# Kernel tuning notes

Measured on AMD Instinct MI355X. Metric: run time of the kernel, lower is better.

Reference implementation:

```python
import jax, jax.numpy as jnp
import numpy as np

T = 256          # tokens
H = 1024         # hidden_size
E = 64           # num_experts
I = 512          # routed intermediate_size
SI = 2048        # shared_expert_intermediate_size
TOP_K = 6
N_GROUP = 8
TOPK_GROUP = 4
ROUTED_SCALE = 2.5


def setup_inputs() -> dict:
    key = jax.random.key(0)
    ks = jax.random.split(key, 9)
    s = 0.02
    return {
        "hidden_states": jax.random.normal(ks[0], (T, H), jnp.float32),
        "gate_w": jax.random.normal(ks[1], (E, H), jnp.float32) * s,
        "e_bias": jax.random.normal(ks[2], (E,), jnp.float32) * 0.01,
        "w1": jax.random.normal(ks[3], (E, I, H), jnp.float32) * s,  # gate proj
        "w3": jax.random.normal(ks[4], (E, I, H), jnp.float32) * s,  # up proj
        "w2": jax.random.normal(ks[5], (E, H, I), jnp.float32) * s,  # down proj
        "ws_gate": jax.random.normal(ks[6], (SI, H), jnp.float32) * s,
        "ws_up": jax.random.normal(ks[7], (SI, H), jnp.float32) * s,
        "ws_down": jax.random.normal(ks[8], (H, SI), jnp.float32) * s,
    }


def _noaux_tc_routing(logits, e_bias):
    # DeepSeek-V3 group-limited sigmoid routing (is_thop=False path).
    scores = jax.nn.sigmoid(logits)                         # [T, E]
    swb = scores + e_bias                                   # bias only picks experts
    t, e = scores.shape
    g = swb.reshape(t, N_GROUP, e // N_GROUP)
    group_scores = jax.lax.top_k(g, 2)[0].sum(-1)           # top-2 sum per group [T, G]
    _, gidx = jax.lax.top_k(group_scores, TOPK_GROUP)
    gmask = jax.nn.one_hot(gidx, N_GROUP, dtype=scores.dtype).sum(-2)  # [T, G]
    smask = jnp.repeat(gmask, e // N_GROUP, axis=-1)        # [T, E]
    _, tidx = jax.lax.top_k(swb * smask, TOP_K)
    nmask = jax.nn.one_hot(tidx, e, dtype=scores.dtype).sum(-2)
    s = scores * nmask
    s = s / (s.sum(-1, keepdims=True) + 1e-20) * ROUTED_SCALE  # [T, E], TOP_K nonzeros
    # torch code returns topk(values, indices) of s; s itself is the dense
    # combine-weight matrix with exactly those values scattered at the indices.
    return s


def reference(hidden_states, gate_w, e_bias, w1, w3, w2, ws_gate, ws_up, ws_down):
    x = hidden_states
    # gate: cublas_mm with fp32 output
    logits = (x @ gate_w.T).astype(jnp.float32)             # [T, E]
    cw = _noaux_tc_routing(logits, e_bias)                  # [T, E] combine weights

    # routed experts: gated MLP per expert, combined by routing weights
    h1 = jnp.einsum('th,eih->tei', x, w1)
    h3 = jnp.einsum('th,eih->tei', x, w3)
    act = jax.nn.silu(h1) * h3                              # [T, E, I]
    eo = jnp.einsum('tei,ehi->teh', act, w2)                # [T, E, H]
    routed = jnp.einsum('teh,te->th', eo, cw.astype(x.dtype))

    # shared experts: GatedMLP
    shared = (jax.nn.silu(x @ ws_gate.T) * (x @ ws_up.T)) @ ws_down.T

    return shared + routed
```

## Files before the change

kernel.cpp:

```cpp
#include <hip/hip_runtime.h>
#include <math.h>

#define T_TOK 256
#define H_DIM 1024
#define E_NUM 64
#define I_DIM 512
#define SI_DIM 2048

#define BN 64
#define BM 32

typedef __attribute__((ext_vector_type(8))) short short8;
typedef __attribute__((ext_vector_type(8))) __bf16 bf16x8;
typedef __attribute__((ext_vector_type(4))) float floatx4;
typedef __attribute__((ext_vector_type(4))) unsigned short ushort4v;
typedef __attribute__((ext_vector_type(8))) unsigned short ushort8;

static __device__ __forceinline__ unsigned short f2bf(float f) {
  unsigned u = __float_as_uint(f);
  u += 0x7FFFu + ((u >> 16) & 1u);
  return (unsigned short)(u >> 16);
}

static __device__ __forceinline__ ushort4v pack4(floatx4 v) {
  ushort4v b;
  b[0] = f2bf(v[0]); b[1] = f2bf(v[1]); b[2] = f2bf(v[2]); b[3] = f2bf(v[3]);
  return b;
}

static __device__ __forceinline__ bf16x8 pack8(floatx4 a, floatx4 b) {
  ushort8 s;
  s[0] = f2bf(a[0]); s[1] = f2bf(a[1]); s[2] = f2bf(a[2]); s[3] = f2bf(a[3]);
  s[4] = f2bf(b[0]); s[5] = f2bf(b[1]); s[6] = f2bf(b[2]); s[7] = f2bf(b[3]);
  union { ushort8 u; bf16x8 v; } cv; cv.u = s;
  return cv.v;
}

static __device__ __forceinline__ floatx4 mfma16(bf16x8 a, bf16x8 b, floatx4 c) {
  return __builtin_amdgcn_mfma_f32_16x16x32_bf16(a, b, c, 0, 0, 0);
}

__global__ __launch_bounds__(256) void gate_route_kernel(
    const float* __restrict__ x, const float* __restrict__ gw,
    const float* __restrict__ ebias, unsigned short* __restrict__ xbf,
    int* __restrict__ cnt, int* __restrict__ tok_list,
    float* __restrict__ wt_list) {
  const int t = blockIdx.x;
  const int j = threadIdx.x;
  __shared__ float xs[H_DIM];
  __shared__ double pd[4 * 64];

  floatx4 v = ((const floatx4*)(x + (size_t)t * H_DIM))[j];
  xs[4 * j + 0] = v[0]; xs[4 * j + 1] = v[1];
  xs[4 * j + 2] = v[2]; xs[4 * j + 3] = v[3];
  ((ushort4v*)(xbf + (size_t)t * H_DIM))[j] = pack4(v);
  __syncthreads();

  const int e = j & 63, ch = j >> 6;
  const float* wr = gw + (size_t)e * H_DIM + ch * 256;
  const float* xc = xs + ch * 256;
  double acc = 0.0;
  for (int i = 0; i < 64; ++i) {
    floatx4 w = ((const floatx4*)wr)[i];
    acc += (double)xc[4 * i + 0] * (double)w[0]
         + (double)xc[4 * i + 1] * (double)w[1]
         + (double)xc[4 * i + 2] * (double)w[2]
         + (double)xc[4 * i + 3] * (double)w[3];
  }
  pd[ch * 64 + e] = acc;
  __syncthreads();

  if (j < 64) {
    const int lane = j;
    const double logit = pd[lane] + pd[64 + lane] + pd[128 + lane] + pd[192 + lane];
    const double score = 1.0 / (1.0 + exp(-logit));
    const double swb = score + (double)ebias[lane];

    double m1 = swb, m2 = -1.0e300;
    #pragma unroll
    for (int d = 1; d < 8; d <<= 1) {
      double o1 = __shfl_xor(m1, d);
      double o2 = __shfl_xor(m2, d);
      double hi = fmax(m1, o1), lo = fmin(m1, o1);
      m1 = hi;
      m2 = fmax(lo, fmax(m2, o2));
    }
    const double gscore = m1 + m2;

    double gs[8];
    #pragma unroll
    for (int g = 0; g < 8; ++g) gs[g] = __shfl(gscore, g << 3);
    unsigned gsel = 0;
    #pragma unroll
    for (int it = 0; it < 4; ++it) {
      int best = 0; double bv = -1.0e300;
      #pragma unroll
      for (int g = 0; g < 8; ++g) {
        bool taken = (gsel >> g) & 1u;
        if (!taken && gs[g] > bv) { bv = gs[g]; best = g; }
      }
      gsel |= 1u << best;
    }

    double key = ((gsel >> (lane >> 3)) & 1u) ? swb : -1.0e300;
    int selected = 0;
    for (int it = 0; it < 6; ++it) {
      double vv = key; int idx = lane;
      #pragma unroll
      for (int d = 1; d < 64; d <<= 1) {
        double ov = __shfl_xor(vv, d);
        int oi = __shfl_xor(idx, d);
        if (ov > vv || (ov == vv && oi < idx)) { vv = ov; idx = oi; }
      }
      if (lane == idx) { selected = 1; key = -1.0e300; }
    }

    double ssum = selected ? score : 0.0;
    #pragma unroll
    for (int d = 1; d < 64; d <<= 1) ssum += __shfl_xor(ssum, d);

    if (selected) {
      float wgt = (float)(score / (ssum + 1e-20) * 2.5);
      int p = atomicAdd(&cnt[lane], 1);
      tok_list[lane * T_TOK + p] = t;
      wt_list[lane * T_TOK + p] = wgt;
    }
  }
}

__global__ __launch_bounds__(256, 2) void routed_gu_kernel(
    const unsigned short* __restrict__ xbf, const float* __restrict__ w1,
    const float* __restrict__ w3, const int* __restrict__ cnt,
    const int* __restrict__ tok_list, unsigned short* __restrict__ act_r) {
  __shared__ __align__(16) char sAB[BM * 1024];

  const int e = blockIdx.x >> 3;
  const int n0 = (blockIdx.x & 7) * BN;
  const int j = threadIdx.x;
  const int wv = j >> 6, lane = j & 63;
  const int q = lane >> 4, c = lane & 15;
  const int kq = q * 8;
  const int ne = cnt[e];
  if (ne <= 0) return;
  const int* tl = tok_list + e * T_TOK;
  unsigned short* ap = act_r + (size_t)e * T_TOK * I_DIM;

  const float* wgR = w1 + ((size_t)e * I_DIM + n0 + wv * 16 + c) * H_DIM;
  const float* wuR = w3 + ((size_t)e * I_DIM + n0 + wv * 16 + c) * H_DIM;

  const int sr = j >> 3, st8 = (j & 7) * 8;
  const int xrs = (sr & 7) << 4;
  const int xr0 = (c & 7) << 4;

  for (int m0 = 0; m0 < ne; m0 += BM) {
    const int tok = (m0 + sr < ne) ? tl[m0 + sr] : tl[m0];
    const unsigned short* aRow = xbf + (size_t)tok * H_DIM;

    floatx4 cg0 = *(const floatx4*)(wgR + kq);
    floatx4 cg1 = *(const floatx4*)(wgR + kq + 4);
    floatx4 cu0 = *(const floatx4*)(wuR + kq);
    floatx4 cu1 = *(const floatx4*)(wuR + kq + 4);

    floatx4 ag0 = (floatx4)0.0f, ag1 = (floatx4)0.0f;
    floatx4 au0 = (floatx4)0.0f, au1 = (floatx4)0.0f;

    for (int half = 0; half < 2; ++half) {
      const int kbase = half * 512;
      __syncthreads();
      #pragma unroll
      for (int i = 0; i < 512; i += 64) {
        const int col = st8 + i;
        *(bf16x8*)(sAB + sr * 1024 + ((2 * col) ^ xrs)) =
            *(const bf16x8*)(aRow + kbase + col);
      }
      __syncthreads();
      for (int kcl = 0; kcl < 512; kcl += 32) {
        const int kc = kbase + kcl;
        bf16x8 bg = pack8(cg0, cg1);
        bf16x8 bu = pack8(cu0, cu1);
        if (kc + 32 < H_DIM) {
          cg0 = *(const floatx4*)(wgR + kc + 32 + kq);
          cg1 = *(const floatx4*)(wgR + kc + 32 + kq + 4);
          cu0 = *(const floatx4*)(wuR + kc + 32 + kq);
          cu1 = *(const floatx4*)(wuR + kc + 32 + kq + 4);
        }
        const int kb = 2 * (kcl + kq);
        bf16x8 a0 = *(const bf16x8*)(sAB + c * 1024 + (kb ^ xr0));
        bf16x8 a1 = *(const bf16x8*)(sAB + (16 + c) * 1024 + (kb ^ xr0));
        ag0 = mfma16(a0, bg, ag0);
        ag1 = mfma16(a1, bg, ag1);
        au0 = mfma16(a0, bu, au0);
        au1 = mfma16(a1, bu, au1);
      }
    }
    #pragma unroll
    for (int s = 0; s < 2; ++s) {
      floatx4 g = s ? ag1 : ag0;
      floatx4 u = s ? au1 : au0;
      #pragma unroll
      for (int r = 0; r < 4; ++r) {
        const int m = m0 + s * 16 + q * 4 + r;
        if (m < ne) {
          float gg = g[r], uu = u[r];
          float a = gg / (1.0f + __expf(-gg)) * uu;
          ap[(size_t)m * I_DIM + n0 + wv * 16 + c] = f2bf(a);
        }
      }
    }
  }
}

__global__ __launch_bounds__(256, 2) void shared_gu_kernel(
    const unsigned short* __restrict__ xbf, const float* __restrict__ wsg,
    const float* __restrict__ wsu, unsigned short* __restrict__ act_s) {
  __shared__ __align__(16) char sAB[BM * 1024];

  const int n0 = (blockIdx.x & 31) * BN;
  const int m0 = (blockIdx.x >> 5) * BM;
  const int j = threadIdx.x;
  const int wv = j >> 6, lane = j & 63;
  const int q = lane >> 4, c = lane & 15;
  const int kq = q * 8;

  const float* wgR = wsg + (size_t)(n0 + wv * 16 + c) * H_DIM;
  const float* wuR = wsu + (size_t)(n0 + wv * 16 + c) * H_DIM;

  const int sr = j >> 3, st8 = (j & 7) * 8;
  const int xrs = (sr & 7) << 4;
  const int xr0 = (c & 7) << 4;
  const unsigned short* aRow = xbf + (size_t)(m0 + sr) * H_DIM;

  floatx4 cg0 = *(const floatx4*)(wgR + kq);
  floatx4 cg1 = *(const floatx4*)(wgR + kq + 4);
  floatx4 cu0 = *(const floatx4*)(wuR + kq);
  floatx4 cu1 = *(const floatx4*)(wuR + kq + 4);

  floatx4 ag0 = (floatx4)0.0f, ag1 = (floatx4)0.0f;
  floatx4 au0 = (floatx4)0.0f, au1 = (floatx4)0.0f;

  for (int half = 0; half < 2; ++half) {
    const int kbase = half * 512;
    __syncthreads();
    #pragma unroll
    for (int i = 0; i < 512; i += 64) {
      const int col = st8 + i;
      *(bf16x8*)(sAB + sr * 1024 + ((2 * col) ^ xrs)) =
          *(const bf16x8*)(aRow + kbase + col);
    }
    __syncthreads();
    for (int kcl = 0; kcl < 512; kcl += 32) {
      const int kc = kbase + kcl;
      bf16x8 bg = pack8(cg0, cg1);
      bf16x8 bu = pack8(cu0, cu1);
      if (kc + 32 < H_DIM) {
        cg0 = *(const floatx4*)(wgR + kc + 32 + kq);
        cg1 = *(const floatx4*)(wgR + kc + 32 + kq + 4);
        cu0 = *(const floatx4*)(wuR + kc + 32 + kq);
        cu1 = *(const floatx4*)(wuR + kc + 32 + kq + 4);
      }
      const int kb = 2 * (kcl + kq);
      bf16x8 a0 = *(const bf16x8*)(sAB + c * 1024 + (kb ^ xr0));
      bf16x8 a1 = *(const bf16x8*)(sAB + (16 + c) * 1024 + (kb ^ xr0));
      ag0 = mfma16(a0, bg, ag0);
      ag1 = mfma16(a1, bg, ag1);
      au0 = mfma16(a0, bu, au0);
      au1 = mfma16(a1, bu, au1);
    }
  }
  #pragma unroll
  for (int s = 0; s < 2; ++s) {
    floatx4 g = s ? ag1 : ag0;
    floatx4 u = s ? au1 : au0;
    #pragma unroll
    for (int r = 0; r < 4; ++r) {
      const int m = m0 + s * 16 + q * 4 + r;
      float gg = g[r], uu = u[r];
      float a = gg / (1.0f + __expf(-gg)) * uu;
      act_s[(size_t)m * SI_DIM + n0 + wv * 16 + c] = f2bf(a);
    }
  }
}

__global__ __launch_bounds__(256, 2) void shared_down_kernel(
    const unsigned short* __restrict__ act_s, const float* __restrict__ wsd,
    float* __restrict__ out) {
  __shared__ __align__(16) char sAB[BM * 1024];

  const int n0 = (blockIdx.x & 15) * BN;
  const int m0 = ((blockIdx.x >> 4) & 7) * BM;
  const int kh = blockIdx.x >> 7;
  const int kbeg = kh * (SI_DIM / 2);
  const int j = threadIdx.x;
  const int wv = j >> 6, lane = j & 63;
  const int q = lane >> 4, c = lane & 15;
  const int kq = q * 8;

  const float* wR = wsd + (size_t)(n0 + wv * 16 + c) * SI_DIM + kbeg;

  const int sr = j >> 3, st8 = (j & 7) * 8;
  const int xrs = (sr & 7) << 4;
  const int xr0 = (c & 7) << 4;
  const unsigned short* aRow = act_s + (size_t)(m0 + sr) * SI_DIM + kbeg;

  floatx4 cw0 = *(const floatx4*)(wR + kq);
  floatx4 cw1 = *(const floatx4*)(wR + kq + 4);

  floatx4 ac0 = (floatx4)0.0f, ac1 = (floatx4)0.0f;
  for (int half = 0; half < 2; ++half) {
    const int kbase = half * 512;
    __syncthreads();
    #pragma unroll
    for (int i = 0; i < 512; i += 64) {
      const int col = st8 + i;
      *(bf16x8*)(sAB + sr * 1024 + ((2 * col) ^ xrs)) =
          *(const bf16x8*)(aRow + kbase + col);
    }
    __syncthreads();
    for (int kcl = 0; kcl < 512; kcl += 32) {
      const int kc = kbase + kcl;
      bf16x8 b = pack8(cw0, cw1);
      if (kc + 32 < SI_DIM / 2) {
        cw0 = *(const floatx4*)(wR + kc + 32 + kq);
        cw1 = *(const floatx4*)(wR + kc + 32 + kq + 4);
      }
      const int kb = 2 * (kcl + kq);
      bf16x8 a0 = *(const bf16x8*)(sAB + c * 1024 + (kb ^ xr0));
      bf16x8 a1 = *(const bf16x8*)(sAB + (16 + c) * 1024 + (kb ^ xr0));
      ac0 = mfma16(a0, b, ac0);
      ac1 = mfma16(a1, b, ac1);
    }
  }
  #pragma unroll
  for (int s = 0; s < 2; ++s) {
    floatx4 d = s ? ac1 : ac0;
    #pragma unroll
    for (int r = 0; r < 4; ++r) {
      const int m = m0 + s * 16 + q * 4 + r;
      atomicAdd(&out[(size_t)m * H_DIM + n0 + wv * 16 + c], d[r]);
    }
  }
}

__global__ __launch_bounds__(256, 2) void routed_down_kernel(
    const unsigned short* __restrict__ act_r, const float* __restrict__ w2,
    const int* __restrict__ cnt, const int* __restrict__ tok_list,
    const float* __restrict__ wt_list, float* __restrict__ out) {
  __shared__ __align__(16) char sAB[BM * 1024];

  const int e = blockIdx.x >> 4;
  const int n0 = (blockIdx.x & 15) * BN;
  const int j = threadIdx.x;
  const int wv = j >> 6, lane = j & 63;
  const int q = lane >> 4, c = lane & 15;
  const int kq = q * 8;
  const int ne = cnt[e];
  if (ne <= 0) return;
  const int* tl = tok_list + e * T_TOK;
  const float* wl = wt_list + e * T_TOK;
  const unsigned short* apb = act_r + (size_t)e * T_TOK * I_DIM;
  const float* wR = w2 + ((size_t)e * H_DIM + n0 + wv * 16 + c) * I_DIM;

  const int sr = j >> 3, st8 = (j & 7) * 8;
  const int xrs = (sr & 7) << 4;
  const int xr0 = (c & 7) << 4;

  for (int m0 = 0; m0 < ne; m0 += BM) {
    __syncthreads();
    {
      int ar = m0 + sr;
      if (ar >= ne) ar = m0;
      const unsigned short* aRow = apb + (size_t)ar * I_DIM;
      #pragma unroll
      for (int i = 0; i < I_DIM; i += 64) {
        const int col = st8 + i;
        *(bf16x8*)(sAB + sr * 1024 + ((2 * col) ^ xrs)) =
            *(const bf16x8*)(aRow + col);
      }
    }
    __syncthreads();

    floatx4 cw0 = *(const floatx4*)(wR + kq);
    floatx4 cw1 = *(const floatx4*)(wR + kq + 4);

    floatx4 ac0 = (floatx4)0.0f, ac1 = (floatx4)0.0f;
    for (int kc = 0; kc < I_DIM; kc += 32) {
      bf16x8 b = pack8(cw0, cw1);
      if (kc + 32 < I_DIM) {
        cw0 = *(const floatx4*)(wR + kc + 32 + kq);
        cw1 = *(const floatx4*)(wR + kc + 32 + kq + 4);
      }
      const int kb = 2 * (kc + kq);
      bf16x8 a0 = *(const bf16x8*)(sAB + c * 1024 + (kb ^ xr0));
      bf16x8 a1 = *(const bf16x8*)(sAB + (16 + c) * 1024 + (kb ^ xr0));
      ac0 = mfma16(a0, b, ac0);
      ac1 = mfma16(a1, b, ac1);
    }
    #pragma unroll
    for (int s = 0; s < 2; ++s) {
      floatx4 d = s ? ac1 : ac0;
      #pragma unroll
      for (int r = 0; r < 4; ++r) {
        const int mi = s * 16 + q * 4 + r;
        if (m0 + mi < ne) {
          atomicAdd(&out[(size_t)tl[m0 + mi] * H_DIM + n0 + wv * 16 + c],
                    d[r] * wl[m0 + mi]);
        }
      }
    }
  }
}

extern "C" void kernel_launch(void* const* d_in, const int* in_sizes, int n_in,
                              void* d_out, int out_size, void* d_ws, size_t ws_size,
                              hipStream_t stream) {
  const float* x   = (const float*)d_in[0];
  const float* gw  = (const float*)d_in[1];
  const float* eb  = (const float*)d_in[2];
  const float* w1  = (const float*)d_in[3];
  const float* w3  = (const float*)d_in[4];
  const float* w2  = (const float*)d_in[5];
  const float* wsg = (const float*)d_in[6];
  const float* wsu = (const float*)d_in[7];
  const float* wsd = (const float*)d_in[8];
  float* out = (float*)d_out;

  char* ws = (char*)d_ws;
  unsigned short* xbf   = (unsigned short*)(ws);
  unsigned short* act_s = (unsigned short*)(ws + 524288);
  int*   cnt            = (int*)(ws + 1572864);
  int*   tok            = (int*)(ws + 1573120);
  float* wt             = (float*)(ws + 1638656);
  unsigned short* act_r = (unsigned short*)(ws + 1704192);

  hipMemsetAsync(cnt, 0, E_NUM * sizeof(int), stream);
  hipMemsetAsync(out, 0, (size_t)T_TOK * H_DIM * sizeof(float), stream);
  gate_route_kernel<<<dim3(T_TOK), dim3(256), 0, stream>>>(x, gw, eb, xbf, cnt, tok, wt);
  routed_gu_kernel<<<dim3(E_NUM * (I_DIM / BN)), dim3(256), 0, stream>>>(xbf, w1, w3, cnt, tok, act_r);
  shared_gu_kernel<<<dim3((SI_DIM / BN) * (T_TOK / BM)), dim3(256), 0, stream>>>(xbf, wsg, wsu, act_s);
  shared_down_kernel<<<dim3((H_DIM / BN) * (T_TOK / BM) * 2), dim3(256), 0, stream>>>(act_s, wsd, out);
  routed_down_kernel<<<dim3(E_NUM * (H_DIM / BN)), dim3(256), 0, stream>>>(act_r, w2, cnt, tok, wt, out);
}
```

Before: 480.6 us.

## Stage converted bf16 weight tiles in LDS and stream activations from global

```diff
diff --git a/kernel.cpp b/kernel.cpp
--- a/kernel.cpp
+++ b/kernel.cpp
@@ -6,15 +6,11 @@
 #define E_NUM 64
 #define I_DIM 512
 #define SI_DIM 2048
-
-#define BN 64
-#define BM 32
-
-typedef __attribute__((ext_vector_type(8))) short short8;
+#define TK 256
+
 typedef __attribute__((ext_vector_type(8))) __bf16 bf16x8;
 typedef __attribute__((ext_vector_type(4))) float floatx4;
 typedef __attribute__((ext_vector_type(4))) unsigned short ushort4v;
-typedef __attribute__((ext_vector_type(8))) unsigned short ushort8;
 
 static __device__ __forceinline__ unsigned short f2bf(float f) {
   unsigned u = __float_as_uint(f);
@@ -26,14 +22,6 @@
   ushort4v b;
   b[0] = f2bf(v[0]); b[1] = f2bf(v[1]); b[2] = f2bf(v[2]); b[3] = f2bf(v[3]);
   return b;
-}
-
-static __device__ __forceinline__ bf16x8 pack8(floatx4 a, floatx4 b) {
-  ushort8 s;
-  s[0] = f2bf(a[0]); s[1] = f2bf(a[1]); s[2] = f2bf(a[2]); s[3] = f2bf(a[3]);
-  s[4] = f2bf(b[0]); s[5] = f2bf(b[1]); s[6] = f2bf(b[2]); s[7] = f2bf(b[3]);
-  union { ushort8 u; bf16x8 v; } cv; cv.u = s;
-  return cv.v;
 }
 
 static __device__ __forceinline__ floatx4 mfma16(bf16x8 a, bf16x8 b, floatx4 c) {
@@ -128,14 +116,15 @@
   }
 }
 
-__global__ __launch_bounds__(256, 2) void routed_gu_kernel(
+__global__ __launch_bounds__(256, 4) void routed_gu_kernel(
     const unsigned short* __restrict__ xbf, const float* __restrict__ w1,
     const float* __restrict__ w3, const int* __restrict__ cnt,
     const int* __restrict__ tok_list, unsigned short* __restrict__ act_r) {
-  __shared__ __align__(16) char sAB[BM * 1024];
-
-  const int e = blockIdx.x >> 3;
-  const int n0 = (blockIdx.x & 7) * BN;
+  __shared__ __align__(16) char sW[2 * 32 * 512];
+
+  const int bid = blockIdx.x;
+  const int e = bid >> 4;
+  const int n0 = (bid & 15) * 32;
   const int j = threadIdx.x;
   const int wv = j >> 6, lane = j & 63;
   const int q = lane >> 4, c = lane & 15;
@@ -145,210 +134,190 @@
   const int* tl = tok_list + e * T_TOK;
   unsigned short* ap = act_r + (size_t)e * T_TOK * I_DIM;
 
-  const float* wgR = w1 + ((size_t)e * I_DIM + n0 + wv * 16 + c) * H_DIM;
-  const float* wuR = w3 + ((size_t)e * I_DIM + n0 + wv * 16 + c) * H_DIM;
-
-  const int sr = j >> 3, st8 = (j & 7) * 8;
-  const int xrs = (sr & 7) << 4;
-  const int xr0 = (c & 7) << 4;
-
-  for (int m0 = 0; m0 < ne; m0 += BM) {
-    const int tok = (m0 + sr < ne) ? tl[m0 + sr] : tl[m0];
-    const unsigned short* aRow = xbf + (size_t)tok * H_DIM;
-
-    floatx4 cg0 = *(const floatx4*)(wgR + kq);
-    floatx4 cg1 = *(const floatx4*)(wgR + kq + 4);
-    floatx4 cu0 = *(const floatx4*)(wuR + kq);
-    floatx4 cu1 = *(const floatx4*)(wuR + kq + 4);
-
-    floatx4 ag0 = (floatx4)0.0f, ag1 = (floatx4)0.0f;
-    floatx4 au0 = (floatx4)0.0f, au1 = (floatx4)0.0f;
-
-    for (int half = 0; half < 2; ++half) {
-      const int kbase = half * 512;
+  const float* w1g = w1 + ((size_t)e * I_DIM + n0) * H_DIM;
+  const float* w3g = w3 + ((size_t)e * I_DIM + n0) * H_DIM;
+  const int x0 = (c & 7) << 4;
+
+  for (int m0 = 0; m0 < ne; m0 += 64) {
+    int ti = m0 + wv * 16 + c; if (ti > ne - 1) ti = ne - 1;
+    const unsigned short* aP = xbf + (size_t)tl[ti] * H_DIM;
+
+    floatx4 ag0 = (floatx4)0.f, ag1 = (floatx4)0.f;
+    floatx4 au0 = (floatx4)0.f, au1 = (floatx4)0.f;
+
+    for (int kt = 0; kt < H_DIM; kt += TK) {
       __syncthreads();
       #pragma unroll
-      for (int i = 0; i < 512; i += 64) {
-        const int col = st8 + i;
-        *(bf16x8*)(sAB + sr * 1024 + ((2 * col) ^ xrs)) =
-            *(const bf16x8*)(aRow + kbase + col);
+      for (int b = 0; b < 2; ++b) {
+        floatx4 f[8];
+        #pragma unroll
+        for (int t = 0; t < 8; ++t) {
+          const int id = wv * 16 + b * 8 + t;
+          const float* base = (id < 32) ? w1g : w3g;
+          f[t] = *(const floatx4*)(base + (size_t)(id & 31) * H_DIM + kt + lane * 4);
+        }
+        #pragma unroll
+        for (int t = 0; t < 8; ++t) {
+          const int id = wv * 16 + b * 8 + t;
+          const int rl = id & 31;
+          *(ushort4v*)(sW + (id >> 5) * 16384 + rl * 512 +
+                       ((lane * 8) ^ ((rl & 7) << 4))) = pack4(f[t]);
+        }
       }
       __syncthreads();
-      for (int kcl = 0; kcl < 512; kcl += 32) {
-        const int kc = kbase + kcl;
-        bf16x8 bg = pack8(cg0, cg1);
-        bf16x8 bu = pack8(cu0, cu1);
-        if (kc + 32 < H_DIM) {
-          cg0 = *(const floatx4*)(wgR + kc + 32 + kq);
-          cg1 = *(const floatx4*)(wgR + kc + 32 + kq + 4);
-          cu0 = *(const floatx4*)(wuR + kc + 32 + kq);
-          cu1 = *(const floatx4*)(wuR + kc + 32 + kq + 4);
-        }
+      for (int kcl = 0; kcl < TK; kcl += 32) {
+        bf16x8 a = *(const bf16x8*)(aP + kt + kcl + kq);
         const int kb = 2 * (kcl + kq);
-        bf16x8 a0 = *(const bf16x8*)(sAB + c * 1024 + (kb ^ xr0));
-        bf16x8 a1 = *(const bf16x8*)(sAB + (16 + c) * 1024 + (kb ^ xr0));
-        ag0 = mfma16(a0, bg, ag0);
-        ag1 = mfma16(a1, bg, ag1);
-        au0 = mfma16(a0, bu, au0);
-        au1 = mfma16(a1, bu, au1);
-      }
-    }
-    #pragma unroll
-    for (int s = 0; s < 2; ++s) {
-      floatx4 g = s ? ag1 : ag0;
-      floatx4 u = s ? au1 : au0;
-      #pragma unroll
-      for (int r = 0; r < 4; ++r) {
-        const int m = m0 + s * 16 + q * 4 + r;
-        if (m < ne) {
-          float gg = g[r], uu = u[r];
-          float a = gg / (1.0f + __expf(-gg)) * uu;
-          ap[(size_t)m * I_DIM + n0 + wv * 16 + c] = f2bf(a);
-        }
-      }
-    }
-  }
-}
-
-__global__ __launch_bounds__(256, 2) void shared_gu_kernel(
+        bf16x8 bg0 = *(const bf16x8*)(sW + c * 512 + (kb ^ x0));
+        bf16x8 bg1 = *(const bf16x8*)(sW + (16 + c) * 512 + (kb ^ x0));
+        bf16x8 bu0 = *(const bf16x8*)(sW + 16384 + c * 512 + (kb ^ x0));
+        bf16x8 bu1 = *(const bf16x8*)(sW + 16384 + (16 + c) * 512 + (kb ^ x0));
+        ag0 = mfma16(a, bg0, ag0);
+        ag1 = mfma16(a, bg1, ag1);
+        au0 = mfma16(a, bu0, au0);
+        au1 = mfma16(a, bu1, au1);
+      }
+    }
+    #pragma unroll
+    for (int r = 0; r < 4; ++r) {
+      const int m = m0 + wv * 16 + q * 4 + r;
+      if (m < ne) {
+        float g0 = ag0[r], u0 = au0[r];
+        float g1 = ag1[r], u1 = au1[r];
+        ap[(size_t)m * I_DIM + n0 + c] = f2bf(g0 / (1.f + __expf(-g0)) * u0);
+        ap[(size_t)m * I_DIM + n0 + 16 + c] = f2bf(g1 / (1.f + __expf(-g1)) * u1);
+      }
+    }
+  }
+}
+
+__global__ __launch_bounds__(256, 4) void shared_gu_kernel(
     const unsigned short* __restrict__ xbf, const float* __restrict__ wsg,
     const float* __restrict__ wsu, unsigned short* __restrict__ act_s) {
-  __shared__ __align__(16) char sAB[BM * 1024];
-
-  const int n0 = (blockIdx.x & 31) * BN;
-  const int m0 = (blockIdx.x >> 5) * BM;
+  __shared__ __align__(16) char sW[2 * 32 * 512];
+
+  const int bid = blockIdx.x;
+  const int n0 = (bid & 63) * 32;
+  const int m0 = (bid >> 6) * 64;
   const int j = threadIdx.x;
   const int wv = j >> 6, lane = j & 63;
   const int q = lane >> 4, c = lane & 15;
   const int kq = q * 8;
 
-  const float* wgR = wsg + (size_t)(n0 + wv * 16 + c) * H_DIM;
-  const float* wuR = wsu + (size_t)(n0 + wv * 16 + c) * H_DIM;
-
-  const int sr = j >> 3, st8 = (j & 7) * 8;
-  const int xrs = (sr & 7) << 4;
-  const int xr0 = (c & 7) << 4;
-  const unsigned short* aRow = xbf + (size_t)(m0 + sr) * H_DIM;
-
-  floatx4 cg0 = *(const floatx4*)(wgR + kq);
-  floatx4 cg1 = *(const floatx4*)(wgR + kq + 4);
-  floatx4 cu0 = *(const floatx4*)(wuR + kq);
-  floatx4 cu1 = *(const floatx4*)(wuR + kq + 4);
-
-  floatx4 ag0 = (floatx4)0.0f, ag1 = (floatx4)0.0f;
-  floatx4 au0 = (floatx4)0.0f, au1 = (floatx4)0.0f;
-
-  for (int half = 0; half < 2; ++half) {
-    const int kbase = half * 512;
+  const float* wgg = wsg + (size_t)n0 * H_DIM;
+  const float* wug = wsu + (size_t)n0 * H_DIM;
+  const int x0 = (c & 7) << 4;
+  const unsigned short* aP = xbf + (size_t)(m0 + wv * 16 + c) * H_DIM;
+
+  floatx4 ag0 = (floatx4)0.f, ag1 = (floatx4)0.f;
+  floatx4 au0 = (floatx4)0.f, au1 = (floatx4)0.f;
+
+  for (int kt = 0; kt < H_DIM; kt += TK) {
     __syncthreads();
     #pragma unroll
-    for (int i = 0; i < 512; i += 64) {
-      const int col = st8 + i;
-      *(bf16x8*)(sAB + sr * 1024 + ((2 * col) ^ xrs)) =
-          *(const bf16x8*)(aRow + kbase + col);
+    for (int b = 0; b < 2; ++b) {
+      floatx4 f[8];
+      #pragma unroll
+      for (int t = 0; t < 8; ++t) {
+        const int id = wv * 16 + b * 8 + t;
+        const float* base = (id < 32) ? wgg : wug;
+        f[t] = *(const floatx4*)(base + (size_t)(id & 31) * H_DIM + kt + lane * 4);
+      }
+      #pragma unroll
+      for (int t = 0; t < 8; ++t) {
+        const int id = wv * 16 + b * 8 + t;
+        const int rl = id & 31;
+        *(ushort4v*)(sW + (id >> 5) * 16384 + rl * 512 +
+                     ((lane * 8) ^ ((rl & 7) << 4))) = pack4(f[t]);
+      }
     }
     __syncthreads();
-    for (int kcl = 0; kcl < 512; kcl += 32) {
-      const int kc = kbase + kcl;
-      bf16x8 bg = pack8(cg0, cg1);
-      bf16x8 bu = pack8(cu0, cu1);
-      if (kc + 32 < H_DIM) {
-        cg0 = *(const floatx4*)(wgR + kc + 32 + kq);
-        cg1 = *(const floatx4*)(wgR + kc + 32 + kq + 4);
-        cu0 = *(const floatx4*)(wuR + kc + 32 + kq);
-        cu1 = *(const floatx4*)(wuR + kc + 32 + kq + 4);
-      }
+    for (int kcl = 0; kcl < TK; kcl += 32) {
+      bf16x8 a = *(const bf16x8*)(aP + kt + kcl + kq);
       const int kb = 2 * (kcl + kq);
-      bf16x8 a0 = *(const bf16x8*)(sAB + c * 1024 + (kb ^ xr0));
-      bf16x8 a1 = *(const bf16x8*)(sAB + (16 + c) * 1024 + (kb ^ xr0));
-      ag0 = mfma16(a0, bg, ag0);
-      ag1 = mfma16(a1, bg, ag1);
-      au0 = mfma16(a0, bu, au0);
-      au1 = mfma16(a1, bu, au1);
+      bf16x8 bg0 = *(const bf16x8*)(sW + c * 512 + (kb ^ x0));
+      bf16x8 bg1 = *(const bf16x8*)(sW + (16 + c) * 512 + (kb ^ x0));
+      bf16x8 bu0 = *(const bf16x8*)(sW + 16384 + c * 512 + (kb ^ x0));
+      bf16x8 bu1 = *(const bf16x8*)(sW + 16384 + (16 + c) * 512 + (kb ^ x0));
+      ag0 = mfma16(a, bg0, ag0);
+      ag1 = mfma16(a, bg1, ag1);
+      au0 = mfma16(a, bu0, au0);
+      au1 = mfma16(a, bu1, au1);
     }
   }
   #pragma unroll
-  for (int s = 0; s < 2; ++s) {
-    floatx4 g = s ? ag1 : ag0;
-    floatx4 u = s ? au1 : au0;
-    #pragma unroll
-    for (int r = 0; r < 4; ++r) {
-      const int m = m0 + s * 16 + q * 4 + r;
-      float gg = g[r], uu = u[r];
-      float a = gg / (1.0f + __expf(-gg)) * uu;
-      act_s[(size_t)m * SI_DIM + n0 + wv * 16 + c] = f2bf(a);
-    }
-  }
-}
-
-__global__ __launch_bounds__(256, 2) void shared_down_kernel(
+  for (int r = 0; r < 4; ++r) {
+    const int m = m0 + wv * 16 + q * 4 + r;
+    float g0 = ag0[r], u0 = au0[r];
+    float g1 = ag1[r], u1 = au1[r];
+    act_s[(size_t)m * SI_DIM + n0 + c] = f2bf(g0 / (1.f + __expf(-g0)) * u0);
+    act_s[(size_t)m * SI_DIM + n0 + 16 + c] = f2bf(g1 / (1.f + __expf(-g1)) * u1);
+  }
+}
+
+__global__ __launch_bounds__(256, 4) void shared_down_kernel(
     const unsigned short* __restrict__ act_s, const float* __restrict__ wsd,
     float* __restrict__ out) {
-  __shared__ __align__(16) char sAB[BM * 1024];
-
-  const int n0 = (blockIdx.x & 15) * BN;
-  const int m0 = ((blockIdx.x >> 4) & 7) * BM;
-  const int kh = blockIdx.x >> 7;
-  const int kbeg = kh * (SI_DIM / 2);
+  __shared__ __align__(16) char sW[32 * 512];
+
+  const int bid = blockIdx.x;
+  const int n0 = (bid & 31) * 32;
+  const int m0 = ((bid >> 5) & 3) * 64;
+  const int kh = bid >> 7;
+  const int k0 = kh * (SI_DIM / 2);
   const int j = threadIdx.x;
   const int wv = j >> 6, lane = j & 63;
   const int q = lane >> 4, c = lane & 15;
   const int kq = q * 8;
 
-  const float* wR = wsd + (size_t)(n0 + wv * 16 + c) * SI_DIM + kbeg;
-
-  const int sr = j >> 3, st8 = (j & 7) * 8;
-  const int xrs = (sr & 7) << 4;
-  const int xr0 = (c & 7) << 4;
-  const unsigned short* aRow = act_s + (size_t)(m0 + sr) * SI_DIM + kbeg;
-
-  floatx4 cw0 = *(const floatx4*)(wR + kq);
-  floatx4 cw1 = *(const floatx4*)(wR + kq + 4);
-
-  floatx4 ac0 = (floatx4)0.0f, ac1 = (floatx4)0.0f;
-  for (int half = 0; half < 2; ++half) {
-    const int kbase = half * 512;
+  const float* wg = wsd + (size_t)n0 * SI_DIM + k0;
+  const int x0 = (c & 7) << 4;
+  const unsigned short* aP = act_s + (size_t)(m0 + wv * 16 + c) * SI_DIM + k0;
+
+  floatx4 ac0 = (floatx4)0.f, ac1 = (floatx4)0.f;
+
+  for (int kt = 0; kt < SI_DIM / 2; kt += TK) {
     __syncthreads();
-    #pragma unroll
-    for (int i = 0; i < 512; i += 64) {
-      const int col = st8 + i;
-      *(bf16x8*)(sAB + sr * 1024 + ((2 * col) ^ xrs)) =
-          *(const bf16x8*)(aRow + kbase + col);
+    {
+      floatx4 f[8];
+      #pragma unroll
+      for (int t = 0; t < 8; ++t) {
+        const int id = wv * 8 + t;
+        f[t] = *(const floatx4*)(wg + (size_t)id * SI_DIM + kt + lane * 4);
+      }
+      #pragma unroll
+      for (int t = 0; t < 8; ++t) {
+        const int id = wv * 8 + t;
+        *(ushort4v*)(sW + id * 512 + ((lane * 8) ^ ((id & 7) << 4))) = pack4(f[t]);
+      }
     }
     __syncthreads();
-    for (int kcl = 0; kcl < 512; kcl += 32) {
-      const int kc = kbase + kcl;
-      bf16x8 b = pack8(cw0, cw1);
-      if (kc + 32 < SI_DIM / 2) {
-        cw0 = *(const floatx4*)(wR + kc + 32 + kq);
-        cw1 = *(const floatx4*)(wR + kc + 32 + kq + 4);
-      }
+    for (int kcl = 0; kcl < TK; kcl += 32) {
+      bf16x8 a = *(const bf16x8*)(aP + kt + kcl + kq);
       const int kb = 2 * (kcl + kq);
-      bf16x8 a0 = *(const bf16x8*)(sAB + c * 1024 + (kb ^ xr0));
-      bf16x8 a1 = *(const bf16x8*)(sAB + (16 + c) * 1024 + (kb ^ xr0));
-      ac0 = mfma16(a0, b, ac0);
-      ac1 = mfma16(a1, b, ac1);
+      bf16x8 b0 = *(const bf16x8*)(sW + c * 512 + (kb ^ x0));
+      bf16x8 b1 = *(const bf16x8*)(sW + (16 + c) * 512 + (kb ^ x0));
+      ac0 = mfma16(a, b0, ac0);
+      ac1 = mfma16(a, b1, ac1);
     }
   }
   #pragma unroll
-  for (int s = 0; s < 2; ++s) {
-    floatx4 d = s ? ac1 : ac0;
-    #pragma unroll
-    for (int r = 0; r < 4; ++r) {
-      const int m = m0 + s * 16 + q * 4 + r;
-      atomicAdd(&out[(size_t)m * H_DIM + n0 + wv * 16 + c], d[r]);
-    }
-  }
-}
-
-__global__ __launch_bounds__(256, 2) void routed_down_kernel(
+  for (int r = 0; r < 4; ++r) {
+    const int m = m0 + wv * 16 + q * 4 + r;
+    atomicAdd(&out[(size_t)m * H_DIM + n0 + c], ac0[r]);
+    atomicAdd(&out[(size_t)m * H_DIM + n0 + 16 + c], ac1[r]);
+  }
+}
+
+__global__ __launch_bounds__(256, 4) void routed_down_kernel(
     const unsigned short* __restrict__ act_r, const float* __restrict__ w2,
     const int* __restrict__ cnt, const int* __restrict__ tok_list,
     const float* __restrict__ wt_list, float* __restrict__ out) {
-  __shared__ __align__(16) char sAB[BM * 1024];
-
-  const int e = blockIdx.x >> 4;
-  const int n0 = (blockIdx.x & 15) * BN;
+  __shared__ __align__(16) char sW[32 * 512];
+
+  const int bid = blockIdx.x;
+  const int e = bid >> 5;
+  const int n0 = (bid & 31) * 32;
   const int j = threadIdx.x;
   const int wv = j >> 6, lane = j & 63;
   const int q = lane >> 4, c = lane & 15;
@@ -358,53 +327,48 @@
   const int* tl = tok_list + e * T_TOK;
   const float* wl = wt_list + e * T_TOK;
   const unsigned short* apb = act_r + (size_t)e * T_TOK * I_DIM;
-  const float* wR = w2 + ((size_t)e * H_DIM + n0 + wv * 16 + c) * I_DIM;
-
-  const int sr = j >> 3, st8 = (j & 7) * 8;
-  const int xrs = (sr & 7) << 4;
-  const int xr0 = (c & 7) << 4;
-
-  for (int m0 = 0; m0 < ne; m0 += BM) {
-    __syncthreads();
-    {
-      int ar = m0 + sr;
-      if (ar >= ne) ar = m0;
-      const unsigned short* aRow = apb + (size_t)ar * I_DIM;
-      #pragma unroll
-      for (int i = 0; i < I_DIM; i += 64) {
-        const int col = st8 + i;
-        *(bf16x8*)(sAB + sr * 1024 + ((2 * col) ^ xrs)) =
-            *(const bf16x8*)(aRow + col);
-      }
-    }
-    __syncthreads();
-
-    floatx4 cw0 = *(const floatx4*)(wR + kq);
-    floatx4 cw1 = *(const floatx4*)(wR + kq + 4);
-
-    floatx4 ac0 = (floatx4)0.0f, ac1 = (floatx4)0.0f;
-    for (int kc = 0; kc < I_DIM; kc += 32) {
-      bf16x8 b = pack8(cw0, cw1);
-      if (kc + 32 < I_DIM) {
-        cw0 = *(const floatx4*)(wR + kc + 32 + kq);
-        cw1 = *(const floatx4*)(wR + kc + 32 + kq + 4);
-      }
-      const int kb = 2 * (kc + kq);
-      bf16x8 a0 = *(const bf16x8*)(sAB + c * 1024 + (kb ^ xr0));
-      bf16x8 a1 = *(const bf16x8*)(sAB + (16 + c) * 1024 + (kb ^ xr0));
-      ac0 = mfma16(a0, b, ac0);
-      ac1 = mfma16(a1, b, ac1);
-    }
-    #pragma unroll
-    for (int s = 0; s < 2; ++s) {
-      floatx4 d = s ? ac1 : ac0;
-      #pragma unroll
-      for (int r = 0; r < 4; ++r) {
-        const int mi = s * 16 + q * 4 + r;
-        if (m0 + mi < ne) {
-          atomicAdd(&out[(size_t)tl[m0 + mi] * H_DIM + n0 + wv * 16 + c],
-                    d[r] * wl[m0 + mi]);
+  const float* wg = w2 + ((size_t)e * H_DIM + n0) * I_DIM;
+  const int x0 = (c & 7) << 4;
+
+  for (int m0 = 0; m0 < ne; m0 += 64) {
+    int mi_ = m0 + wv * 16 + c; if (mi_ > ne - 1) mi_ = ne - 1;
+    const unsigned short* aP = apb + (size_t)mi_ * I_DIM;
+
+    floatx4 ac0 = (floatx4)0.f, ac1 = (floatx4)0.f;
+
+    for (int kt = 0; kt < I_DIM; kt += TK) {
+      __syncthreads();
+      {
+        floatx4 f[8];
+        #pragma unroll
+        for (int t = 0; t < 8; ++t) {
+          const int id = wv * 8 + t;
+          f[t] = *(const floatx4*)(wg + (size_t)id * I_DIM + kt + lane * 4);
         }
+        #pragma unroll
+        for (int t = 0; t < 8; ++t) {
+          const int id = wv * 8 + t;
+          *(ushort4v*)(sW + id * 512 + ((lane * 8) ^ ((id & 7) << 4))) = pack4(f[t]);
+        }
+      }
+      __syncthreads();
+      for (int kcl = 0; kcl < TK; kcl += 32) {
+        bf16x8 a = *(const bf16x8*)(aP + kt + kcl + kq);
+        const int kb = 2 * (kcl + kq);
+        bf16x8 b0 = *(const bf16x8*)(sW + c * 512 + (kb ^ x0));
+        bf16x8 b1 = *(const bf16x8*)(sW + (16 + c) * 512 + (kb ^ x0));
+        ac0 = mfma16(a, b0, ac0);
+        ac1 = mfma16(a, b1, ac1);
+      }
+    }
+    #pragma unroll
+    for (int r = 0; r < 4; ++r) {
+      const int m = m0 + wv * 16 + q * 4 + r;
+      if (m < ne) {
+        const float w = wl[m];
+        float* o = out + (size_t)tl[m] * H_DIM + n0;
+        atomicAdd(o + c, ac0[r] * w);
+        atomicAdd(o + 16 + c, ac1[r] * w);
       }
     }
   }
@@ -435,8 +399,8 @@
   hipMemsetAsync(cnt, 0, E_NUM * sizeof(int), stream);
   hipMemsetAsync(out, 0, (size_t)T_TOK * H_DIM * sizeof(float), stream);
   gate_route_kernel<<<dim3(T_TOK), dim3(256), 0, stream>>>(x, gw, eb, xbf, cnt, tok, wt);
-  routed_gu_kernel<<<dim3(E_NUM * (I_DIM / BN)), dim3(256), 0, stream>>>(xbf, w1, w3, cnt, tok, act_r);
-  shared_gu_kernel<<<dim3((SI_DIM / BN) * (T_TOK / BM)), dim3(256), 0, stream>>>(xbf, wsg, wsu, act_s);
-  shared_down_kernel<<<dim3((H_DIM / BN) * (T_TOK / BM) * 2), dim3(256), 0, stream>>>(act_s, wsd, out);
-  routed_down_kernel<<<dim3(E_NUM * (H_DIM / BN)), dim3(256), 0, stream>>>(act_r, w2, cnt, tok, wt, out);
-}
+  routed_gu_kernel<<<dim3(E_NUM * (I_DIM / 32)), dim3(256), 0, stream>>>(xbf, w1, w3, cnt, tok, act_r);
+  shared_gu_kernel<<<dim3((SI_DIM / 32) * (T_TOK / 64)), dim3(256), 0, stream>>>(xbf, wsg, wsu, act_s);
+  shared_down_kernel<<<dim3(32 * 4 * 2), dim3(256), 0, stream>>>(act_s, wsd, out);
+  routed_down_kernel<<<dim3(E_NUM * (H_DIM / 32)), dim3(256), 0, stream>>>(act_r, w2, cnt, tok, wt, out);
+}
```

Result: faster. 448.8 us (-6.6%).
